# Kernel tuning notes

Hardware: AMD Instinct MI355X
Metric: run time of the kernel (lower is better)

Reference implementation:

```python
import jax, jax.numpy as jnp
import numpy as np

N, C = 1048576, 128
GAMMA = 2.0
SMOOTHING = 0.1


def setup_inputs() -> dict:
    key = jax.random.key(0)
    k1, k2, k3, k4, k5 = jax.random.split(key, 5)
    inputs = jax.random.normal(k1, (N, C), dtype=jnp.float32)
    targets = jax.random.randint(k2, (N,), 0, C)
    class_weights = jax.random.uniform(k3, (C,), minval=0.5, maxval=2.0, dtype=jnp.float32)
    hot = (jax.random.uniform(k4, (C, C)) > 0.9).astype(jnp.float32)
    extra = jax.random.uniform(k5, (C, C), minval=0.0, maxval=2.0, dtype=jnp.float32)
    penalty_matrix = 1.0 + hot * extra
    penalty_matrix = penalty_matrix * (1.0 - jnp.eye(C, dtype=jnp.float32)) + jnp.eye(C, dtype=jnp.float32)
    return {"inputs": inputs, "targets": targets,
            "class_weights": class_weights, "penalty_matrix": penalty_matrix}


def reference(inputs, targets, class_weights, penalty_matrix):
    num_classes = inputs.shape[-1]
    # label smoothing on one-hot targets
    one_hot = jax.nn.one_hot(targets, num_classes, dtype=inputs.dtype)  # [N, C]
    smooth_targets = one_hot * (1.0 - SMOOTHING) + SMOOTHING / num_classes
    log_probs = jax.nn.log_softmax(inputs, axis=-1)  # [N, C]
    probs = jnp.exp(log_probs)
    focal_weights = (1.0 - probs) ** GAMMA
    base_loss = -(focal_weights * smooth_targets * log_probs).sum(axis=-1)  # [N]
    base_loss = base_loss * class_weights[targets]
    # confusion penalty: sum_{j != t} max(P[t, j] - 1, 0) * probs[:, j]
    # (original loop only adds when p > 1.0 and skips j == i)
    excess = jnp.maximum(penalty_matrix - 1.0, 0.0)
    excess = excess * (1.0 - jnp.eye(num_classes, dtype=inputs.dtype))
    confusion_penalty = (excess[targets] * probs).sum(axis=-1)  # [N]
    return (base_loss + confusion_penalty).mean()
```

## Files before the change

### kernel.cpp

```cpp
#include <hip/hip_runtime.h>


#define NROWS 1048576
#define NCLS  128
#define BLOCK 256
#define GRID  4096

constexpr float SMOOTH_OFF = 0.1f / 128.0f;
constexpr float SMOOTH_ON  = 0.9f;

__global__ __launch_bounds__(BLOCK) void focal_main(
    const float* __restrict__ inputs,
    const int*   __restrict__ targets,
    const float* __restrict__ cls_w,
    const float* __restrict__ P,
    float*       __restrict__ partial)
{
    const int tid   = threadIdx.x;
    const int lane  = tid & 63;
    const int wib   = tid >> 6;
    const int sub   = lane & 31;
    const int half  = lane >> 5;
    const int wavesPerBlk = BLOCK / 64;

    const long long waveId   = (long long)blockIdx.x * wavesPerBlk + wib;
    const long long numWaves = (long long)GRID * wavesPerBlk;
    const long long numPairs = NROWS / 2;

    float acc = 0.0f;

    for (long long pair = waveId; pair < numPairs; pair += numWaves) {
        const size_t row = (size_t)pair * 2 + half;

        const float4 v = ((const float4*)(inputs + row * NCLS))[sub];
        float xv[4] = {v.x, v.y, v.z, v.w};

        float m = fmaxf(fmaxf(xv[0], xv[1]), fmaxf(xv[2], xv[3]));
        #pragma unroll
        for (int off = 16; off > 0; off >>= 1)
            m = fmaxf(m, __shfl_xor(m, off, 64));

        float ev[4];
        #pragma unroll
        for (int k = 0; k < 4; ++k) ev[k] = __expf(xv[k] - m);

        float z = (ev[0] + ev[1]) + (ev[2] + ev[3]);
        #pragma unroll
        for (int off = 16; off > 0; off >>= 1)
            z += __shfl_xor(z, off, 64);

        const float logZ = __logf(z);
        const float rZ   = 1.0f / z;

        const int   t  = targets[row];
        const float cw = cls_w[t];
        const float4 prv = ((const float4*)(P + (size_t)t * NCLS))[sub];
        float pv[4] = {prv.x, prv.y, prv.z, prv.w};

        const int jbase = sub * 4;
        float base = 0.0f, pen = 0.0f;
        #pragma unroll
        for (int k = 0; k < 4; ++k) {
            const float lp = xv[k] - m - logZ;
            const float p  = ev[k] * rZ;
            const float om = 1.0f - p;
            const float fw = om * om;
            const float sm = SMOOTH_OFF + ((jbase + k == t) ? SMOOTH_ON : 0.0f);
            base -= fw * sm * lp;
            pen  += fmaxf(pv[k] - 1.0f, 0.0f) * p;
        }
        acc += cw * base + pen;
    }

    #pragma unroll
    for (int off = 32; off > 0; off >>= 1)
        acc += __shfl_xor(acc, off, 64);

    __shared__ float ssum[BLOCK / 64];
    if (lane == 0) ssum[wib] = acc;
    __syncthreads();
    if (tid == 0) {
        float s = 0.0f;
        #pragma unroll
        for (int w = 0; w < BLOCK / 64; ++w) s += ssum[w];
        partial[blockIdx.x] = s;
    }
}

__global__ __launch_bounds__(256) void focal_final(
    const float* __restrict__ partial, float* __restrict__ out)
{
    double s = 0.0;
    for (int i = threadIdx.x; i < GRID; i += 256) s += (double)partial[i];

    #pragma unroll
    for (int off = 32; off > 0; off >>= 1)
        s += __shfl_xor(s, off, 64);

    __shared__ double sh[4];
    const int wave = threadIdx.x >> 6;
    if ((threadIdx.x & 63) == 0) sh[wave] = s;
    __syncthreads();
    if (threadIdx.x == 0) {
        double tot = sh[0] + sh[1] + sh[2] + sh[3];
        out[0] = (float)(tot / (double)NROWS);
    }
}

extern "C" void kernel_launch(void* const* d_in, const int* in_sizes, int n_in,
                              void* d_out, int out_size, void* d_ws, size_t ws_size,
                              hipStream_t stream) {
    const float* inputs  = (const float*)d_in[0];
    const int*   targets = (const int*)  d_in[1];
    const float* cls_w   = (const float*)d_in[2];
    const float* P       = (const float*)d_in[3];
    float* out     = (float*)d_out;
    float* partial = (float*)d_ws;

    focal_main<<<GRID, BLOCK, 0, stream>>>(inputs, targets, cls_w, P, partial);
    focal_final<<<1, 256, 0, stream>>>(partial, out);
}
```

Measured before the change: 693.5 us.

## Process four rows per wave with register prefetch and nontemporal loads

Reworks the main loop so each wave handles four rows per iteration (16 lanes per row, 8 floats per lane) over a contiguous chunk instead of a grid-strided pair. The next quad's inputs and targets are software-prefetched into registers while the current one is computed, and input loads use nontemporal hints. The smoothed-target sum is also factored algebraically to cut per-element multiplies. The cost is higher register pressure and an extra wasted prefetch at the end of each chunk, which wraps to the first quad.

```diff
diff --git a/kernel.cpp b/kernel.cpp
--- a/kernel.cpp
+++ b/kernel.cpp
@@ -6,8 +6,15 @@
 #define BLOCK 256
 #define GRID  4096
 
+#define WPB    (BLOCK / 64)
+#define NWAVES (GRID * WPB)
+#define NQUADS (NROWS / 4)
+#define QPW    (NQUADS / NWAVES)
+
 constexpr float SMOOTH_OFF = 0.1f / 128.0f;
 constexpr float SMOOTH_ON  = 0.9f;
+
+using f4 = __attribute__((ext_vector_type(4))) float;
 
 __global__ __launch_bounds__(BLOCK) void focal_main(
     const float* __restrict__ inputs,
@@ -16,73 +23,87 @@
     const float* __restrict__ P,
     float*       __restrict__ partial)
 {
-    const int tid   = threadIdx.x;
-    const int lane  = tid & 63;
-    const int wib   = tid >> 6;
-    const int sub   = lane & 31;
-    const int half  = lane >> 5;
-    const int wavesPerBlk = BLOCK / 64;
+    const int tid  = threadIdx.x;
+    const int lane = tid & 63;
+    const int wib  = tid >> 6;
+    const int g    = lane >> 4;
+    const int q16  = lane & 15;
+    const int jb   = q16 * 8;
 
-    const long long waveId   = (long long)blockIdx.x * wavesPerBlk + wib;
-    const long long numWaves = (long long)GRID * wavesPerBlk;
-    const long long numPairs = NROWS / 2;
+    const int waveId = blockIdx.x * WPB + wib;
+    const f4* in4 = reinterpret_cast<const f4*>(inputs);
+
+    int q = waveId * QPW;
+
+    f4 A = __builtin_nontemporal_load(in4 + (size_t)q * 128 + lane * 2);
+    f4 B = __builtin_nontemporal_load(in4 + (size_t)q * 128 + lane * 2 + 1);
+    int t = targets[q * 4 + g];
 
     float acc = 0.0f;
 
-    for (long long pair = waveId; pair < numPairs; pair += numWaves) {
-        const size_t row = (size_t)pair * 2 + half;
+    for (int it = 0; it < QPW; ++it) {
+        int qn = q + 1;
+        if (qn >= NQUADS) qn = 0;
+        const f4 An = __builtin_nontemporal_load(in4 + (size_t)qn * 128 + lane * 2);
+        const f4 Bn = __builtin_nontemporal_load(in4 + (size_t)qn * 128 + lane * 2 + 1);
+        const int tn = targets[qn * 4 + g];
 
-        const float4 v = ((const float4*)(inputs + row * NCLS))[sub];
-        float xv[4] = {v.x, v.y, v.z, v.w};
+        const float cw = cls_w[t];
+        const f4* prow = reinterpret_cast<const f4*>(P + (size_t)t * NCLS);
+        const f4 pa = prow[q16 * 2];
+        const f4 pb = prow[q16 * 2 + 1];
 
-        float m = fmaxf(fmaxf(xv[0], xv[1]), fmaxf(xv[2], xv[3]));
+        float m = fmaxf(fmaxf(fmaxf(A[0], A[1]), fmaxf(A[2], A[3])),
+                        fmaxf(fmaxf(B[0], B[1]), fmaxf(B[2], B[3])));
         #pragma unroll
-        for (int off = 16; off > 0; off >>= 1)
+        for (int off = 8; off > 0; off >>= 1)
             m = fmaxf(m, __shfl_xor(m, off, 64));
 
-        float ev[4];
+        float ev[8];
         #pragma unroll
-        for (int k = 0; k < 4; ++k) ev[k] = __expf(xv[k] - m);
+        for (int k = 0; k < 4; ++k) ev[k]     = __expf(A[k] - m);
+        #pragma unroll
+        for (int k = 0; k < 4; ++k) ev[4 + k] = __expf(B[k] - m);
 
-        float z = (ev[0] + ev[1]) + (ev[2] + ev[3]);
+        float z = ((ev[0] + ev[1]) + (ev[2] + ev[3]))
+                + ((ev[4] + ev[5]) + (ev[6] + ev[7]));
         #pragma unroll
-        for (int off = 16; off > 0; off >>= 1)
+        for (int off = 8; off > 0; off >>= 1)
             z += __shfl_xor(z, off, 64);
 
-        const float logZ = __logf(z);
-        const float rZ   = 1.0f / z;
+        const float mlz = m + __logf(z);
+        const float rZ  = 1.0f / z;
 
-        const int   t  = targets[row];
-        const float cw = cls_w[t];
-        const float4 prv = ((const float4*)(P + (size_t)t * NCLS))[sub];
-        float pv[4] = {prv.x, prv.y, prv.z, prv.w};
+        float s1 = 0.0f, te = 0.0f, pen = 0.0f;
+        #pragma unroll
+        for (int k = 0; k < 8; ++k) {
+            const float x   = (k < 4) ? A[k] : B[k - 4];
+            const float pvk = (k < 4) ? pa[k] : pb[k - 4];
+            const float lp  = x - mlz;
+            const float p   = ev[k] * rZ;
+            const float om  = 1.0f - p;
+            const float fw  = om * om;
+            const float fl  = fw * lp;
+            s1 += fl;
+            if (jb + k == t) te = fl;
+            pen += fmaxf(pvk - 1.0f, 0.0f) * p;
+        }
+        acc += pen - cw * (SMOOTH_OFF * s1 + SMOOTH_ON * te);
 
-        const int jbase = sub * 4;
-        float base = 0.0f, pen = 0.0f;
-        #pragma unroll
-        for (int k = 0; k < 4; ++k) {
-            const float lp = xv[k] - m - logZ;
-            const float p  = ev[k] * rZ;
-            const float om = 1.0f - p;
-            const float fw = om * om;
-            const float sm = SMOOTH_OFF + ((jbase + k == t) ? SMOOTH_ON : 0.0f);
-            base -= fw * sm * lp;
-            pen  += fmaxf(pv[k] - 1.0f, 0.0f) * p;
-        }
-        acc += cw * base + pen;
+        A = An; B = Bn; t = tn; q = qn;
     }
 
     #pragma unroll
     for (int off = 32; off > 0; off >>= 1)
         acc += __shfl_xor(acc, off, 64);
 
-    __shared__ float ssum[BLOCK / 64];
+    __shared__ float ssum[WPB];
     if (lane == 0) ssum[wib] = acc;
     __syncthreads();
     if (tid == 0) {
         float s = 0.0f;
         #pragma unroll
-        for (int w = 0; w < BLOCK / 64; ++w) s += ssum[w];
+        for (int w = 0; w < WPB; ++w) s += ssum[w];
         partial[blockIdx.x] = s;
     }
 }
```

Result: no change. 695.8 us (+0.3%).
